# Optimization experiments

Measured on AMD Instinct MI355X. Metric: run time of the kernel, lower is better.

The kernel has to match this reference:

```python
import jax, jax.numpy as jnp
import numpy as np

N = 50000
IN_DIM, HID, LAT = 128, 256, 64
E = 800000


def setup_inputs() -> dict:
    key = jax.random.key(0)
    ks = jax.random.split(key, 12)
    x = jax.random.normal(ks[0], (N, IN_DIM), dtype=jnp.float32)
    edge_index = jax.random.randint(ks[1], (2, E), 0, N, dtype=jnp.int64)
    edge_weight = jax.random.uniform(ks[2], (E,), dtype=jnp.float32)
    def w(k, i, o):
        return jax.random.normal(k, (i, o), dtype=jnp.float32) * 0.05
    return {
        "x": x, "edge_index": edge_index, "edge_weight": edge_weight,
        "W1": w(ks[3], IN_DIM, HID), "b1": jnp.zeros((HID,), jnp.float32),
        "W2": w(ks[4], HID, LAT),    "b2": jnp.zeros((LAT,), jnp.float32),
        "W3": w(ks[5], LAT, HID),    "b3": jnp.zeros((HID,), jnp.float32),
        "W4": w(ks[6], HID, IN_DIM), "b4": jnp.zeros((IN_DIM,), jnp.float32),
    }


def _gcn_norm(edge_index, edge_weight, n):
    # add self loops with weight 1 (PyG GCNConv default), symmetric normalization
    loop = jnp.arange(n, dtype=edge_index.dtype)
    row = jnp.concatenate([edge_index[0], loop])
    col = jnp.concatenate([edge_index[1], loop])
    ew = jnp.concatenate([edge_weight, jnp.ones((n,), edge_weight.dtype)])
    deg = jax.ops.segment_sum(ew, col, num_segments=n)  # [N]
    dinv = jnp.where(deg > 0, jax.lax.rsqrt(deg), 0.0)
    norm = dinv[row] * ew * dinv[col]                   # [E+N]
    return row, col, norm


def _gcn_conv(x, row, col, norm, W, b, n):
    h = x @ W                                           # [N, out]
    msg = h[row] * norm[:, None]                        # gather + scale [E+N, out]
    out = jax.ops.segment_sum(msg, col, num_segments=n) # scatter-add
    return out + b


def reference(x, edge_index, edge_weight, W1, b1, W2, b2, W3, b3, W4, b4):
    n = x.shape[0]
    row, col, norm = _gcn_norm(edge_index, edge_weight, n)
    # encode (dropout is identity in eval mode)
    h = jax.nn.relu(_gcn_conv(x, row, col, norm, W1, b1, n))
    z = _gcn_conv(h, row, col, norm, W2, b2, n)
    # decode
    h = jax.nn.relu(_gcn_conv(z, row, col, norm, W3, b3, n))
    x_recon = _gcn_conv(h, row, col, norm, W4, b4, n)
    return x_recon
```

## Files before the change

### kernel.cpp

```cpp
#include <hip/hip_runtime.h>
#include <hip/hip_fp16.h>

#define IN_DIM 128
#define HID    256
#define LAT    64

typedef __attribute__((ext_vector_type(8))) short bf16x8;
typedef __attribute__((ext_vector_type(4))) float f32x4;

__device__ __forceinline__ short f2bf(float f) {
    union { float f; unsigned u; } v; v.f = f;
    unsigned r = v.u + 0x7fffu + ((v.u >> 16) & 1u);
    return (short)(r >> 16);
}
__device__ __forceinline__ float bf2f(short s) {
    union { unsigned u; float f; } v; v.u = ((unsigned)(unsigned short)s) << 16;
    return v.f;
}

__device__ __forceinline__ void storeP(__half* p, float v) { *p = __float2half(v); }
__device__ __forceinline__ void storeP(float*  p, float v) { *p = v; }


#define FIXSCALE 1048576.0f

__global__ void k_init(unsigned long long* __restrict__ packed, int n) {
    int i = blockIdx.x * 256 + threadIdx.x;
    if (i < n) packed[i] = (unsigned long long)(1u << 20);
}

__global__ void k_edge_acc(const int* __restrict__ ei, const float* __restrict__ ew,
                           unsigned long long* __restrict__ packed,
                           int* __restrict__ rank, int E) {
    int e = blockIdx.x * 256 + threadIdx.x;
    if (e < E) {
        int c = ei[E + e];
        unsigned fx = (unsigned)lrintf(ew[e] * FIXSCALE);
        unsigned long long old =
            atomicAdd(&packed[c], ((unsigned long long)1 << 40) | (unsigned long long)fx);
        rank[e] = (int)(old >> 40);
    }
}

__global__ void k_derive(const unsigned long long* __restrict__ packed,
                         float* __restrict__ dinv, int* __restrict__ counts, int n) {
    int i = blockIdx.x * 256 + threadIdx.x;
    if (i < n) {
        unsigned long long p = packed[i];
        float deg = (float)(p & (((unsigned long long)1 << 40) - 1)) * (1.0f / FIXSCALE);
        dinv[i]   = rsqrtf(deg);
        counts[i] = (int)(p >> 40);
    }
}

__global__ __launch_bounds__(1024) void k_blocksum(const int* __restrict__ counts,
                                                   int* __restrict__ bsum, int n) {
    __shared__ int ws[16];
    const int t = threadIdx.x, lane = t & 63, wv = t >> 6;
    int i = blockIdx.x * 1024 + t;
    int v = (i < n) ? counts[i] : 0;
    #pragma unroll
    for (int d = 1; d < 64; d <<= 1) v += __shfl_xor(v, d);
    if (lane == 0) ws[wv] = v;
    __syncthreads();
    if (wv == 0 && lane < 16) {
        int x = ws[lane];
        #pragma unroll
        for (int d = 1; d < 16; d <<= 1) x += __shfl_xor(x, d, 16);
        if (lane == 0) bsum[blockIdx.x] = x;
    }
}

__global__ void k_scan_bsums(int* __restrict__ bsum, int nb,
                             int* __restrict__ offsets, int n) {
    int lane = threadIdx.x;
    int v = (lane < nb) ? bsum[lane] : 0;
    #pragma unroll
    for (int d = 1; d < 64; d <<= 1) {
        int u = __shfl_up(v, d);
        if (lane >= d) v += u;
    }
    if (lane < nb) bsum[lane] = v;
    if (lane == nb - 1) offsets[n] = v;
}

__global__ __launch_bounds__(1024) void k_scan_apply(const int* __restrict__ counts,
                                                     const int* __restrict__ bsum,
                                                     int* __restrict__ offsets, int n) {
    __shared__ int ws[16];
    const int t = threadIdx.x, lane = t & 63, wv = t >> 6;
    int i = blockIdx.x * 1024 + t;
    int v = (i < n) ? counts[i] : 0;
    int s = v;
    #pragma unroll
    for (int d = 1; d < 64; d <<= 1) {
        int u = __shfl_up(s, d);
        if (lane >= d) s += u;
    }
    if (lane == 63) ws[wv] = s;
    __syncthreads();
    if (wv == 0 && lane < 16) {
        int x = ws[lane];
        #pragma unroll
        for (int d = 1; d < 16; d <<= 1) {
            int u = __shfl_up(x, d, 16);
            if (lane >= d) x += u;
        }
        ws[lane] = x;
    }
    __syncthreads();
    int base = (blockIdx.x ? bsum[blockIdx.x - 1] : 0) + (wv ? ws[wv - 1] : 0);
    if (i < n) offsets[i] = base + s - v;
}

__global__ void k_fill(const int* __restrict__ ei, const float* __restrict__ ew,
                       const float* __restrict__ dinv, const int* __restrict__ offsets,
                       const int* __restrict__ rank,
                       int2* __restrict__ csr, int E) {
    int e = blockIdx.x * 256 + threadIdx.x;
    if (e < E) {
        int r = ei[e];
        int c = ei[E + e];
        int pos = offsets[c] + rank[e];
        float nm = dinv[r] * ew[e] * dinv[c];
        csr[pos] = make_int2(r, __float_as_int(nm));
    }
}

__global__ void k_cast(const float* __restrict__ x, __half* __restrict__ xh, int total) {
    int idx = (blockIdx.x * 256 + threadIdx.x) * 8;
    if (idx < total) {
        float4 a = *(const float4*)&x[idx];
        float4 b = *(const float4*)&x[idx + 4];
        short4 s0 = make_short4(__half_as_short(__float2half(a.x)), __half_as_short(__float2half(a.y)),
                                __half_as_short(__float2half(a.z)), __half_as_short(__float2half(a.w)));
        short4 s1 = make_short4(__half_as_short(__float2half(b.x)), __half_as_short(__float2half(b.y)),
                                __half_as_short(__float2half(b.z)), __half_as_short(__float2half(b.w)));
        *(short4*)&xh[idx]     = s0;
        *(short4*)&xh[idx + 4] = s1;
    }
}

__global__ void k_splitW_all(const float* __restrict__ W1, short2* __restrict__ S1, int n1,
                             const float* __restrict__ W2, short2* __restrict__ S2, int n2,
                             const float* __restrict__ W3, short2* __restrict__ S3, int n3,
                             const float* __restrict__ W4, short2* __restrict__ S4, int n4) {
    int idx = blockIdx.x * 256 + threadIdx.x;
    const float* W; short2* S;
    if (idx < n1)                { W = W1; S = S1; }
    else if (idx < n1 + n2)      { W = W2; S = S2; idx -= n1; }
    else if (idx < n1 + n2 + n3) { W = W3; S = S3; idx -= n1 + n2; }
    else if (idx < n1 + n2 + n3 + n4) { W = W4; S = S4; idx -= n1 + n2 + n3; }
    else return;
    float w = W[idx];
    short h = f2bf(w);
    short l = f2bf(w - bf2f(h));
    S[idx] = make_short2(h, l);
}

template <int BN, typename PT, bool EPI>
__global__ __launch_bounds__(256) void gemm_mfma(const float* __restrict__ A,
                                                 const short2* __restrict__ Wsp,
                                                 const float* __restrict__ bias,
                                                 PT* __restrict__ P,
                                                 int M, int K, int F) {
    constexpr int WC = BN / 32;
    __shared__ alignas(16) short Ahi[128][40];
    __shared__ alignas(16) short Alo[128][40];
    __shared__ alignas(16) short Whi[BN][40];
    __shared__ alignas(16) short Wlo[BN][40];

    const int bm  = blockIdx.x * 128;
    const int bn  = blockIdx.y * BN;
    const int tid = threadIdx.x;
    const int wv  = tid >> 6;
    const int wy  = wv >> 1;
    const int wx  = wv & 1;
    const int lane = tid & 63;
    const int frow = lane & 15;
    const int fk   = (lane >> 4) * 8;

    const int wc_ = tid % BN;
    const int kg  = tid / BN;
    constexpr int KC = 32 * BN / 256;

    f32x4 acc[4][WC];
    #pragma unroll
    for (int i = 0; i < 4; ++i)
        #pragma unroll
        for (int j = 0; j < WC; ++j)
            acc[i][j] = (f32x4){0.f, 0.f, 0.f, 0.f};

    for (int k0 = 0; k0 < K; k0 += 32) {
        if (k0) __syncthreads();
        #pragma unroll
        for (int it = 0; it < 4; ++it) {
            int l   = tid + it * 256;
            int row = l >> 3;
            int k4  = l & 7;
            int gr  = bm + row;
            float4 v = make_float4(0.f, 0.f, 0.f, 0.f);
            if (gr < M) v = *(const float4*)&A[(size_t)gr * K + k0 + k4 * 4];
            float vv[4] = {v.x, v.y, v.z, v.w};
            short h[4], lo[4];
            #pragma unroll
            for (int j = 0; j < 4; ++j) {
                h[j]  = f2bf(vv[j]);
                lo[j] = f2bf(vv[j] - bf2f(h[j]));
            }
            *(short4*)&Ahi[row][k4 * 4] = make_short4(h[0], h[1], h[2], h[3]);
            *(short4*)&Alo[row][k4 * 4] = make_short4(lo[0], lo[1], lo[2], lo[3]);
        }
        #pragma unroll
        for (int kk = 0; kk < KC; kk += 4) {
            short h[4], lo[4];
            #pragma unroll
            for (int j = 0; j < 4; ++j) {
                short2 hl = Wsp[(size_t)(k0 + kg * KC + kk + j) * F + bn + wc_];
                h[j] = hl.x; lo[j] = hl.y;
            }
            *(short4*)&Whi[wc_][kg * KC + kk] = make_short4(h[0], h[1], h[2], h[3]);
            *(short4*)&Wlo[wc_][kg * KC + kk] = make_short4(lo[0], lo[1], lo[2], lo[3]);
        }
        __syncthreads();
        bf16x8 ah[4], al[4], wh[WC], wl[WC];
        #pragma unroll
        for (int ar = 0; ar < 4; ++ar) {
            ah[ar] = *(const bf16x8*)&Ahi[wy * 64 + ar * 16 + frow][fk];
            al[ar] = *(const bf16x8*)&Alo[wy * 64 + ar * 16 + frow][fk];
        }
        #pragma unroll
        for (int wc = 0; wc < WC; ++wc) {
            wh[wc] = *(const bf16x8*)&Whi[wx * (BN / 2) + wc * 16 + frow][fk];
            wl[wc] = *(const bf16x8*)&Wlo[wx * (BN / 2) + wc * 16 + frow][fk];
        }
        #pragma unroll
        for (int ar = 0; ar < 4; ++ar)
            #pragma unroll
            for (int wc = 0; wc < WC; ++wc) {
                acc[ar][wc] = __builtin_amdgcn_mfma_f32_16x16x32_bf16(ah[ar], wh[wc], acc[ar][wc], 0, 0, 0);
                acc[ar][wc] = __builtin_amdgcn_mfma_f32_16x16x32_bf16(ah[ar], wl[wc], acc[ar][wc], 0, 0, 0);
                acc[ar][wc] = __builtin_amdgcn_mfma_f32_16x16x32_bf16(al[ar], wh[wc], acc[ar][wc], 0, 0, 0);
            }
    }
    #pragma unroll
    for (int ar = 0; ar < 4; ++ar)
        #pragma unroll
        for (int r = 0; r < 4; ++r) {
            int row = bm + wy * 64 + ar * 16 + (lane >> 4) * 4 + r;
            if (row >= M) continue;
            #pragma unroll
            for (int wc = 0; wc < WC; ++wc) {
                int col = bn + wx * (BN / 2) + wc * 16 + (lane & 15);
                float o = acc[ar][wc][r];
                if (EPI) o = fmaxf(o + bias[col], 0.f);
                storeP(&P[(size_t)row * F + col], o);
            }
        }
}


template <int VEC>
__device__ __forceinline__ void pload(float* d, const __half* s) {
    if constexpr (VEC == 4) {
        union { short4 s4; __half h[4]; } u;
        u.s4 = *(const short4*)s;
        #pragma unroll
        for (int j = 0; j < 4; ++j) d[j] = __half2float(u.h[j]);
    } else if constexpr (VEC == 2) {
        union { short2 s2; __half h[2]; } u;
        u.s2 = *(const short2*)s;
        d[0] = __half2float(u.h[0]); d[1] = __half2float(u.h[1]);
    } else {
        d[0] = __half2float(*s);
    }
}
template <int VEC>
__device__ __forceinline__ void pload(float* d, const float* s) {
    if constexpr (VEC == 4) { float4 v = *(const float4*)s; d[0]=v.x; d[1]=v.y; d[2]=v.z; d[3]=v.w; }
    else if constexpr (VEC == 2) { float2 v = *(const float2*)s; d[0]=v.x; d[1]=v.y; }
    else { d[0] = *s; }
}
template <int VEC>
__device__ __forceinline__ void pstore(__half* d, const float* s) {
    if constexpr (VEC == 4) {
        *(short4*)d = make_short4(__half_as_short(__float2half(s[0])), __half_as_short(__float2half(s[1])),
                                  __half_as_short(__float2half(s[2])), __half_as_short(__float2half(s[3])));
    } else if constexpr (VEC == 2) {
        *(short2*)d = make_short2(__half_as_short(__float2half(s[0])), __half_as_short(__float2half(s[1])));
    } else {
        *d = __float2half(s[0]);
    }
}
template <int VEC>
__device__ __forceinline__ void pstore(float* d, const float* s) {
    if constexpr (VEC == 4) { *(float4*)d = make_float4(s[0], s[1], s[2], s[3]); }
    else if constexpr (VEC == 2) { *(float2*)d = make_float2(s[0], s[1]); }
    else { *d = s[0]; }
}

template <int VEC, bool HASB, typename TN, typename TS, typename TOUT>
__global__ __launch_bounds__(256) void agg_kernel(
    const TN* __restrict__ pre, const TS* __restrict__ self,
    const float* __restrict__ bias,
    const int* __restrict__ offsets, const int2* __restrict__ csr,
    const float* __restrict__ dinv, TOUT* __restrict__ out, int n) {
    constexpr int F = VEC * 64;
    const int wave = threadIdx.x >> 6;
    const int lane = threadIdx.x & 63;
    const int c = blockIdx.x * 4 + wave;
    if (c >= n) return;
    const float di = dinv[c];
    const float sn = di * di;
    float acc[VEC];
    pload<VEC>(acc, self + (size_t)c * F + lane * VEC);
    #pragma unroll
    for (int v = 0; v < VEC; ++v) acc[v] *= sn;
    const int beg = offsets[c], end = offsets[c + 1];
    int j = beg;
    for (; j + 7 < end; j += 8) {
        int2 e[8];
        #pragma unroll
        for (int q = 0; q < 8; ++q) e[q] = csr[j + q];
        float t[8][VEC];
        #pragma unroll
        for (int q = 0; q < 8; ++q)
            pload<VEC>(t[q], pre + (size_t)e[q].x * F + lane * VEC);
        #pragma unroll
        for (int q = 0; q < 8; ++q)
            #pragma unroll
            for (int v = 0; v < VEC; ++v)
                acc[v] = fmaf(__int_as_float(e[q].y), t[q][v], acc[v]);
    }
    for (; j + 3 < end; j += 4) {
        int2 e[4];
        #pragma unroll
        for (int q = 0; q < 4; ++q) e[q] = csr[j + q];
        float t[4][VEC];
        #pragma unroll
        for (int q = 0; q < 4; ++q)
            pload<VEC>(t[q], pre + (size_t)e[q].x * F + lane * VEC);
        #pragma unroll
        for (int q = 0; q < 4; ++q)
            #pragma unroll
            for (int v = 0; v < VEC; ++v)
                acc[v] = fmaf(__int_as_float(e[q].y), t[q][v], acc[v]);
    }
    for (; j < end; ++j) {
        int2 e0 = csr[j];
        float t0[VEC];
        pload<VEC>(t0, pre + (size_t)e0.x * F + lane * VEC);
        #pragma unroll
        for (int v = 0; v < VEC; ++v) acc[v] = fmaf(__int_as_float(e0.y), t0[v], acc[v]);
    }
    if (HASB) {
        float bv[VEC];
        pload<VEC>(bv, bias + lane * VEC);
        #pragma unroll
        for (int v = 0; v < VEC; ++v) acc[v] += bv[v];
    }
    pstore<VEC>(out + (size_t)c * F + lane * VEC, acc);
}


extern "C" void kernel_launch(void* const* d_in, const int* in_sizes, int n_in,
                              void* d_out, int out_size, void* d_ws, size_t ws_size,
                              hipStream_t stream) {
    const float* x  = (const float*)d_in[0];
    const int*   ei = (const int*)  d_in[1];
    const float* ew = (const float*)d_in[2];
    const float* W1 = (const float*)d_in[3];
    const float* b1 = (const float*)d_in[4];
    const float* W2 = (const float*)d_in[5];
    const float* b2 = (const float*)d_in[6];
    const float* W3 = (const float*)d_in[7];
    const float* b3 = (const float*)d_in[8];
    const float* W4 = (const float*)d_in[9];
    const float* b4 = (const float*)d_in[10];

    const int N = in_sizes[0] / IN_DIM;
    const int E = in_sizes[2];

    char* p = (char*)d_ws;
    auto alloc = [&](size_t bytes) -> void* {
        void* r = (void*)p;
        p += (bytes + 255) & ~(size_t)255;
        return r;
    };
    unsigned long long* packed = (unsigned long long*)alloc((size_t)N * 8);
    float*  dinv     = (float*)alloc((size_t)N * 4);
    int*    counts   = (int*)  alloc((size_t)N * 4);
    int*    offsets  = (int*)  alloc((size_t)(N + 1) * 4);
    int*    bsum     = (int*)  alloc((size_t)64 * 4);
    int*    rank     = (int*)  alloc((size_t)E * 4);
    int2*   csr      = (int2*) alloc((size_t)E * 8);
    short2* Wsp1     = (short2*)alloc((size_t)IN_DIM * HID * 4);
    short2* Wsp2     = (short2*)alloc((size_t)HID * LAT * 4);
    short2* Wsp3     = (short2*)alloc((size_t)LAT * HID * 4);
    short2* Wsp4     = (short2*)alloc((size_t)HID * IN_DIM * 4);
    __half* xh       = (__half*)alloc((size_t)N * IN_DIM * 2);
    float*  ha       = (float*) alloc((size_t)N * IN_DIM * 4);
    float*  h        = (float*) alloc((size_t)N * HID * 4);
    __half* P2       = (__half*)alloc((size_t)N * LAT * 2);
    __half* zh       = (__half*)alloc((size_t)N * LAT * 2);
    float*  za       = (float*)xh;
    float*  P4       = ha;
    __half* P4h      = xh;

    const int gN  = (N + 255) / 256;
    const int gE  = (E + 255) / 256;
    const int nbS = (N + 1023) / 1024;
    const int nbM = (N + 127) / 128;
    const int nodeBlocks = (N + 3) / 4;
    const int castBlocks = (N * IN_DIM / 8 + 255) / 256;
    const int nW = IN_DIM * HID + HID * LAT + LAT * HID + HID * IN_DIM;

    k_init      <<<gN, 256, 0, stream>>>(packed, N);
    k_edge_acc  <<<gE, 256, 0, stream>>>(ei, ew, packed, rank, E);
    k_derive    <<<gN, 256, 0, stream>>>(packed, dinv, counts, N);
    k_blocksum  <<<nbS, 1024, 0, stream>>>(counts, bsum, N);
    k_scan_bsums<<<1, 64, 0, stream>>>(bsum, nbS, offsets, N);
    k_scan_apply<<<nbS, 1024, 0, stream>>>(counts, bsum, offsets, N);
    k_fill      <<<gE, 256, 0, stream>>>(ei, ew, dinv, offsets, rank, csr, E);
    k_cast      <<<castBlocks, 256, 0, stream>>>(x, xh, N * IN_DIM);
    k_splitW_all<<<(nW + 255) / 256, 256, 0, stream>>>(
        W1, Wsp1, IN_DIM * HID, W2, Wsp2, HID * LAT,
        W3, Wsp3, LAT * HID,   W4, Wsp4, HID * IN_DIM);

    agg_kernel<2, false, __half, __half, float><<<nodeBlocks, 256, 0, stream>>>(xh, xh, nullptr, offsets, csr, dinv, ha, N);
    gemm_mfma<128, float, true><<<dim3(nbM, HID / 128), 256, 0, stream>>>(ha, Wsp1, b1, h, N, IN_DIM, HID);

    gemm_mfma<64, __half, false><<<dim3(nbM, LAT / 64), 256, 0, stream>>>(h, Wsp2, nullptr, P2, N, HID, LAT);
    agg_kernel<1, true, __half, __half, __half><<<nodeBlocks, 256, 0, stream>>>(P2, P2, b2, offsets, csr, dinv, zh, N);

    agg_kernel<1, false, __half, __half, float><<<nodeBlocks, 256, 0, stream>>>(zh, zh, nullptr, offsets, csr, dinv, za, N);
    gemm_mfma<128, float, true><<<dim3(nbM, HID / 128), 256, 0, stream>>>(za, Wsp3, b3, h, N, LAT, HID);

    gemm_mfma<128, float, false><<<dim3(nbM, IN_DIM / 128), 256, 0, stream>>>(h, Wsp4, nullptr, P4, N, HID, IN_DIM);
    k_cast<<<castBlocks, 256, 0, stream>>>(P4, P4h, N * IN_DIM);
    agg_kernel<2, true, __half, float, float><<<nodeBlocks, 256, 0, stream>>>(P4h, P4, b4, offsets, csr, dinv, (float*)d_out, N);
}
```

Baseline: 404.8 us.

## Pre-transpose split bf16 weights and load MFMA fragments directly from global

The weight split kernel now writes separate hi/lo bf16 arrays transposed to [F][K] layout. The GEMM drops its shared-memory weight tiles and lets each lane load its bf16x8 fragments straight from global memory (L2/L1 cached). This removes the scattered short2 staging loads and the LDS writes and reads for weights. In exchange, each wave issues redundant global loads for the same weight fragments, and their latency is now exposed inside the k-loop.

```diff
diff --git a/kernel.cpp b/kernel.cpp
--- a/kernel.cpp
+++ b/kernel.cpp
@@ -141,34 +141,37 @@
     }
 }
 
-__global__ void k_splitW_all(const float* __restrict__ W1, short2* __restrict__ S1, int n1,
-                             const float* __restrict__ W2, short2* __restrict__ S2, int n2,
-                             const float* __restrict__ W3, short2* __restrict__ S3, int n3,
-                             const float* __restrict__ W4, short2* __restrict__ S4, int n4) {
+__global__ void k_splitW_all(
+    const float* __restrict__ W1, short* __restrict__ H1, short* __restrict__ G1, int K1, int F1,
+    const float* __restrict__ W2, short* __restrict__ H2, short* __restrict__ G2, int K2, int F2,
+    const float* __restrict__ W3, short* __restrict__ H3, short* __restrict__ G3, int K3, int F3,
+    const float* __restrict__ W4, short* __restrict__ H4, short* __restrict__ G4, int K4, int F4) {
     int idx = blockIdx.x * 256 + threadIdx.x;
-    const float* W; short2* S;
-    if (idx < n1)                { W = W1; S = S1; }
-    else if (idx < n1 + n2)      { W = W2; S = S2; idx -= n1; }
-    else if (idx < n1 + n2 + n3) { W = W3; S = S3; idx -= n1 + n2; }
-    else if (idx < n1 + n2 + n3 + n4) { W = W4; S = S4; idx -= n1 + n2 + n3; }
+    const int n1 = K1 * F1, n2 = K2 * F2, n3 = K3 * F3, n4 = K4 * F4;
+    const float* W; short* H; short* G; int K, F;
+    if (idx < n1)                          { W = W1; H = H1; G = G1; K = K1; F = F1; }
+    else if (idx < n1 + n2)                { idx -= n1;           W = W2; H = H2; G = G2; K = K2; F = F2; }
+    else if (idx < n1 + n2 + n3)           { idx -= n1 + n2;      W = W3; H = H3; G = G3; K = K3; F = F3; }
+    else if (idx < n1 + n2 + n3 + n4)      { idx -= n1 + n2 + n3; W = W4; H = H4; G = G4; K = K4; F = F4; }
     else return;
+    int k = idx / F, f = idx % F;
     float w = W[idx];
     short h = f2bf(w);
     short l = f2bf(w - bf2f(h));
-    S[idx] = make_short2(h, l);
+    H[(size_t)f * K + k] = h;
+    G[(size_t)f * K + k] = l;
 }
 
 template <int BN, typename PT, bool EPI>
 __global__ __launch_bounds__(256) void gemm_mfma(const float* __restrict__ A,
-                                                 const short2* __restrict__ Wsp,
+                                                 const short* __restrict__ Wth,
+                                                 const short* __restrict__ Wtl,
                                                  const float* __restrict__ bias,
                                                  PT* __restrict__ P,
                                                  int M, int K, int F) {
     constexpr int WC = BN / 32;
     __shared__ alignas(16) short Ahi[128][40];
     __shared__ alignas(16) short Alo[128][40];
-    __shared__ alignas(16) short Whi[BN][40];
-    __shared__ alignas(16) short Wlo[BN][40];
 
     const int bm  = blockIdx.x * 128;
     const int bn  = blockIdx.y * BN;
@@ -180,9 +183,10 @@
     const int frow = lane & 15;
     const int fk   = (lane >> 4) * 8;
 
-    const int wc_ = tid % BN;
-    const int kg  = tid / BN;
-    constexpr int KC = 32 * BN / 256;
+    size_t wbase[WC];
+    #pragma unroll
+    for (int wc = 0; wc < WC; ++wc)
+        wbase[wc] = (size_t)(bn + wx * (BN / 2) + wc * 16 + frow) * K + fk;
 
     f32x4 acc[4][WC];
     #pragma unroll
@@ -211,28 +215,18 @@
             *(short4*)&Ahi[row][k4 * 4] = make_short4(h[0], h[1], h[2], h[3]);
             *(short4*)&Alo[row][k4 * 4] = make_short4(lo[0], lo[1], lo[2], lo[3]);
         }
-        #pragma unroll
-        for (int kk = 0; kk < KC; kk += 4) {
-            short h[4], lo[4];
-            #pragma unroll
-            for (int j = 0; j < 4; ++j) {
-                short2 hl = Wsp[(size_t)(k0 + kg * KC + kk + j) * F + bn + wc_];
-                h[j] = hl.x; lo[j] = hl.y;
-            }
-            *(short4*)&Whi[wc_][kg * KC + kk] = make_short4(h[0], h[1], h[2], h[3]);
-            *(short4*)&Wlo[wc_][kg * KC + kk] = make_short4(lo[0], lo[1], lo[2], lo[3]);
+        bf16x8 wh[WC], wl[WC];
+        #pragma unroll
+        for (int wc = 0; wc < WC; ++wc) {
+            wh[wc] = *(const bf16x8*)&Wth[wbase[wc] + k0];
+            wl[wc] = *(const bf16x8*)&Wtl[wbase[wc] + k0];
         }
         __syncthreads();
-        bf16x8 ah[4], al[4], wh[WC], wl[WC];
+        bf16x8 ah[4], al[4];
         #pragma unroll
         for (int ar = 0; ar < 4; ++ar) {
             ah[ar] = *(const bf16x8*)&Ahi[wy * 64 + ar * 16 + frow][fk];
             al[ar] = *(const bf16x8*)&Alo[wy * 64 + ar * 16 + frow][fk];
-        }
-        #pragma unroll
-        for (int wc = 0; wc < WC; ++wc) {
-            wh[wc] = *(const bf16x8*)&Whi[wx * (BN / 2) + wc * 16 + frow][fk];
-            wl[wc] = *(const bf16x8*)&Wlo[wx * (BN / 2) + wc * 16 + frow][fk];
         }
         #pragma unroll
         for (int ar = 0; ar < 4; ++ar)
@@ -394,10 +388,14 @@
     int*    bsum     = (int*)  alloc((size_t)64 * 4);
     int*    rank     = (int*)  alloc((size_t)E * 4);
     int2*   csr      = (int2*) alloc((size_t)E * 8);
-    short2* Wsp1     = (short2*)alloc((size_t)IN_DIM * HID * 4);
-    short2* Wsp2     = (short2*)alloc((size_t)HID * LAT * 4);
-    short2* Wsp3     = (short2*)alloc((size_t)LAT * HID * 4);
-    short2* Wsp4     = (short2*)alloc((size_t)HID * IN_DIM * 4);
+    short*  Wh1      = (short*)alloc((size_t)IN_DIM * HID * 2);
+    short*  Wl1      = (short*)alloc((size_t)IN_DIM * HID * 2);
+    short*  Wh2      = (short*)alloc((size_t)HID * LAT * 2);
+    short*  Wl2      = (short*)alloc((size_t)HID * LAT * 2);
+    short*  Wh3      = (short*)alloc((size_t)LAT * HID * 2);
+    short*  Wl3      = (short*)alloc((size_t)LAT * HID * 2);
+    short*  Wh4      = (short*)alloc((size_t)HID * IN_DIM * 2);
+    short*  Wl4      = (short*)alloc((size_t)HID * IN_DIM * 2);
     __half* xh       = (__half*)alloc((size_t)N * IN_DIM * 2);
     float*  ha       = (float*) alloc((size_t)N * IN_DIM * 4);
     float*  h        = (float*) alloc((size_t)N * HID * 4);
@@ -424,19 +422,19 @@
     k_fill      <<<gE, 256, 0, stream>>>(ei, ew, dinv, offsets, rank, csr, E);
     k_cast      <<<castBlocks, 256, 0, stream>>>(x, xh, N * IN_DIM);
     k_splitW_all<<<(nW + 255) / 256, 256, 0, stream>>>(
-        W1, Wsp1, IN_DIM * HID, W2, Wsp2, HID * LAT,
-        W3, Wsp3, LAT * HID,   W4, Wsp4, HID * IN_DIM);
+        W1, Wh1, Wl1, IN_DIM, HID,  W2, Wh2, Wl2, HID, LAT,
+        W3, Wh3, Wl3, LAT, HID,     W4, Wh4, Wl4, HID, IN_DIM);
 
     agg_kernel<2, false, __half, __half, float><<<nodeBlocks, 256, 0, stream>>>(xh, xh, nullptr, offsets, csr, dinv, ha, N);
-    gemm_mfma<128, float, true><<<dim3(nbM, HID / 128), 256, 0, stream>>>(ha, Wsp1, b1, h, N, IN_DIM, HID);
-
-    gemm_mfma<64, __half, false><<<dim3(nbM, LAT / 64), 256, 0, stream>>>(h, Wsp2, nullptr, P2, N, HID, LAT);
+    gemm_mfma<128, float, true><<<dim3(nbM, HID / 128), 256, 0, stream>>>(ha, Wh1, Wl1, b1, h, N, IN_DIM, HID);
+
+    gemm_mfma<64, __half, false><<<dim3(nbM, LAT / 64), 256, 0, stream>>>(h, Wh2, Wl2, nullptr, P2, N, HID, LAT);
     agg_kernel<1, true, __half, __half, __half><<<nodeBlocks, 256, 0, stream>>>(P2, P2, b2, offsets, csr, dinv, zh, N);
 
     agg_kernel<1, false, __half, __half, float><<<nodeBlocks, 256, 0, stream>>>(zh, zh, nullptr, offsets, csr, dinv, za, N);
-    gemm_mfma<128, float, true><<<dim3(nbM, HID / 128), 256, 0, stream>>>(za, Wsp3, b3, h, N, LAT, HID);
-
-    gemm_mfma<128, float, false><<<dim3(nbM, IN_DIM / 128), 256, 0, stream>>>(h, Wsp4, nullptr, P4, N, HID, IN_DIM);
+    gemm_mfma<128, float, true><<<dim3(nbM, HID / 128), 256, 0, stream>>>(za, Wh3, Wl3, b3, h, N, LAT, HID);
+
+    gemm_mfma<128, float, false><<<dim3(nbM, IN_DIM / 128), 256, 0, stream>>>(h, Wh4, Wl4, nullptr, P4, N, HID, IN_DIM);
     k_cast<<<castBlocks, 256, 0, stream>>>(P4, P4h, N * IN_DIM);
     agg_kernel<2, true, __half, float, float><<<nodeBlocks, 256, 0, stream>>>(P4h, P4, b4, offsets, csr, dinv, (float*)d_out, N);
 }
```

After: 418.1 us. 3.3% more time.
